# Kernel optimization log

Hardware: AMD Instinct MI355X
Metric: run time of the kernel (lower is better)

The kernel has to match this reference:

```python
import jax, jax.numpy as jnp
import numpy as np

B, N, DIM = 2, 2048, 1024
HEADS, DIM_HEAD = 16, 64
SCALE = DIM_HEAD ** 0.5  # NOTE: original code MULTIPLIES q by sqrt(d)


def setup_inputs() -> dict:
    key = jax.random.key(0)
    k1, k2, k3 = jax.random.split(key, 3)
    x = jax.random.normal(k1, (B, N, DIM), dtype=jnp.float32)
    mask = jnp.ones((B, N), dtype=bool)
    w_qkv = jax.random.normal(k2, (DIM, 3 * HEADS * DIM_HEAD), dtype=jnp.float32) * 0.02
    w_out = jax.random.normal(k3, (HEADS * DIM_HEAD, DIM), dtype=jnp.float32) * 0.02
    return {"x": x, "mask": mask, "w_qkv": w_qkv, "w_out": w_out}


def reference(x, mask, w_qkv, w_out):
    b, n, _ = x.shape
    # qkv projection: b n (qkv h d) -> qkv b h n d
    qkv = (x @ w_qkv).reshape(b, n, 3, HEADS, DIM_HEAD)
    qkv = jnp.transpose(qkv, (2, 0, 3, 1, 4))  # [3, b, h, n, d]
    q, k, v = qkv[0], qkv[1], qkv[2]
    q = q * SCALE
    sim = jnp.einsum('bhid,bhjd->bhij', q, k)
    neg = -jnp.finfo(sim.dtype).max
    sim = jnp.where(mask[:, None, None, :], sim, neg)
    attn = jax.nn.softmax(sim, axis=-1)
    out = jnp.einsum('bhij,bhjd->bhid', attn, v)  # [b, h, n, d]
    out = jnp.transpose(out, (0, 2, 1, 3)).reshape(b, n, HEADS * DIM_HEAD)
    return out @ w_out
```

## Files before the change

kernel.cpp:

```cpp
#include <hip/hip_runtime.h>
#include <hip/hip_bf16.h>

typedef _Float16 f16x8 __attribute__((ext_vector_type(8)));
typedef _Float16 f16x4 __attribute__((ext_vector_type(4)));
typedef float f32x4 __attribute__((ext_vector_type(4)));
typedef unsigned int u32;

#define MFMA16(a, b, c) __builtin_amdgcn_mfma_f32_16x16x32_f16(a, b, c, 0, 0, 0)

#define QSCALE 11.54156032f

__device__ __forceinline__ void gld16(const void* g, void* l) {
  using gp_t = const __attribute__((address_space(1))) u32*;
  using lp_t = __attribute__((address_space(3))) u32*;
  __builtin_amdgcn_global_load_lds((gp_t)g, (lp_t)l, 16, 0, 0);
}

__global__ void conv_f32_f16(const float* __restrict__ in, _Float16* __restrict__ out) {
  int i = (blockIdx.x * 256 + threadIdx.x) * 4;
  float4 v = *(const float4*)(in + i);
  f16x4 h = {(_Float16)v.x, (_Float16)v.y, (_Float16)v.z, (_Float16)v.w};
  *(f16x4*)(out + i) = h;
}

__global__ void transpose_f32_f16(const float* __restrict__ in, _Float16* __restrict__ out,
                                  int R, int C) {
  __shared__ float t[32][33];
  const int tx = threadIdx.x, ty = threadIdx.y;
  const int bx = blockIdx.x * 32, by = blockIdx.y * 32;
  for (int i = 0; i < 32; i += 8)
    t[ty + i][tx] = in[(size_t)(by + ty + i) * C + bx + tx];
  __syncthreads();
  for (int i = 0; i < 32; i += 8)
    out[(size_t)(bx + ty + i) * R + by + tx] = (_Float16)t[tx][ty + i];
}

template <int MODE>
__global__ __launch_bounds__(256) void gemm128(
    const _Float16* __restrict__ A, const _Float16* __restrict__ Bt, int Kd,
    _Float16* __restrict__ qo, _Float16* __restrict__ ko, _Float16* __restrict__ vt,
    float* __restrict__ fo, int Nd) {
  __shared__ __align__(16) _Float16 As[128 * 64];
  __shared__ __align__(16) _Float16 Bs[128 * 64];
  const int tid = threadIdx.x;
  const int w = tid >> 6, l = tid & 63;
  const int wm = w >> 1, wn = w & 1;
  const int lr = l & 15, lg = l >> 4;
  const int nwg = gridDim.x;
  int lin = blockIdx.x;
  lin = (lin & 7) * (nwg >> 3) + (lin >> 3);
  const int m0 = (lin & 31) * 128, n0 = (lin >> 5) * 128;

  const int srow = tid >> 3;
  const int scol = ((tid & 7) ^ (srow & 7)) * 8;
  const int swzr = (lr & 7) << 3;

  f32x4 acc[4][4];
  for (int i = 0; i < 4; ++i)
    for (int j = 0; j < 4; ++j) acc[i][j] = (f32x4){0.f, 0.f, 0.f, 0.f};

  const int NT = Kd >> 6;
  for (int kt = 0; kt < NT; ++kt) {
    const int k0 = kt * 64;
    for (int c = 0; c < 4; ++c) {
      const int row = c * 32 + srow;
      const int lbase = (c * 32 + w * 8) * 64;
      gld16(A + (size_t)(m0 + row) * Kd + k0 + scol, &As[lbase]);
      gld16(Bt + (size_t)(n0 + row) * Kd + k0 + scol, &Bs[lbase]);
    }
    __syncthreads();
    for (int kk = 0; kk < 2; ++kk) {
      f16x8 af[4], bf[4];
      const int cofs = (kk * 32 + lg * 8) ^ swzr;
      for (int mt = 0; mt < 4; ++mt)
        af[mt] = *(const f16x8*)&As[(wm * 64 + mt * 16 + lr) * 64 + cofs];
      for (int nt = 0; nt < 4; ++nt)
        bf[nt] = *(const f16x8*)&Bs[(wn * 64 + nt * 16 + lr) * 64 + cofs];
      for (int mt = 0; mt < 4; ++mt)
        for (int nt = 0; nt < 4; ++nt) acc[mt][nt] = MFMA16(af[mt], bf[nt], acc[mt][nt]);
    }
    __syncthreads();
  }

  for (int mt = 0; mt < 4; ++mt)
    for (int nt = 0; nt < 4; ++nt) {
      const int gmB = m0 + wm * 64 + mt * 16 + lg * 4;
      const int gn = n0 + wn * 64 + nt * 16 + lr;
      for (int r = 0; r < 4; ++r) {
        const int gm = gmB + r;
        const float v = acc[mt][nt][r];
        if (MODE == 0) {
          const int b = gm >> 11, ns = gm & 2047;
          const int sect = gn >> 10, rem = gn & 1023;
          const int h = rem >> 6, d = rem & 63;
          const size_t bh = (size_t)b * 16 + h;
          if (sect == 0)
            qo[(bh * 2048 + ns) * 64 + d] = (_Float16)(v * QSCALE);
          else if (sect == 1)
            ko[(bh * 2048 + ns) * 64 + d] = (_Float16)v;
          else
            vt[(bh * 64 + d) * 2048 + ns] = (_Float16)v;
        } else {
          fo[(size_t)gm * Nd + gn] = v;
        }
      }
    }
}

__global__ __launch_bounds__(256) void attn_kernel(
    const _Float16* __restrict__ Q, const _Float16* __restrict__ K,
    const _Float16* __restrict__ Vt, _Float16* __restrict__ AO) {
  __shared__ __align__(16) _Float16 Kls[64 * 64];
  __shared__ __align__(16) _Float16 Vls[64 * 64];
  __shared__ __align__(16) _Float16 Pls[4 * 16 * 64];
  const int qt = blockIdx.x, bh = blockIdx.y;
  const int b = bh >> 4, h = bh & 15;
  const int tid = threadIdx.x, w = tid >> 6, l = tid & 63;
  const int lr = l & 15, lg = l >> 4;
  const int q0 = qt * 64;
  const int pswz = (lr & 7) << 3;

  f16x8 qf[2];
  {
    const _Float16* qp = Q + ((size_t)bh * 2048 + q0 + w * 16 + lr) * 64 + lg * 8;
    qf[0] = *(const f16x8*)qp;
    qf[1] = *(const f16x8*)(qp + 32);
  }
  float mrun = -INFINITY, lsum = 0.f;
  f32x4 ao[4];
  for (int dt = 0; dt < 4; ++dt) ao[dt] = (f32x4){0.f, 0.f, 0.f, 0.f};

  const int srow = tid >> 2, cb = tid & 3;
  const _Float16* Kbase = K + ((size_t)bh * 2048 + srow) * 64 + cb * 8;
  const _Float16* Vbase = Vt + ((size_t)bh * 64 + srow) * 2048 + cb * 8;
  const int lofs0 = srow * 64 + ((cb ^ (srow & 7)) << 3);
  const int lofs1 = srow * 64 + (((cb + 4) ^ (srow & 7)) << 3);

  f16x8 kr0, kr1, vr0, vr1;
  kr0 = *(const f16x8*)(Kbase);
  kr1 = *(const f16x8*)(Kbase + 32);
  vr0 = *(const f16x8*)(Vbase);
  vr1 = *(const f16x8*)(Vbase + 32);
  *(f16x8*)&Kls[lofs0] = kr0;
  *(f16x8*)&Kls[lofs1] = kr1;
  *(f16x8*)&Vls[lofs0] = vr0;
  *(f16x8*)&Vls[lofs1] = vr1;
  __syncthreads();

  _Float16* pw = &Pls[w * (16 * 64)];
  const int NT = 2048 / 64;
  for (int t = 0; t < NT; ++t) {
    if (t + 1 < NT) {
      const size_t g = (size_t)(t + 1) * 64;
      kr0 = *(const f16x8*)(Kbase + g * 64);
      kr1 = *(const f16x8*)(Kbase + g * 64 + 32);
      vr0 = *(const f16x8*)(Vbase + g);
      vr1 = *(const f16x8*)(Vbase + g + 32);
    }
    f32x4 sc[4];
    for (int ct = 0; ct < 4; ++ct) sc[ct] = (f32x4){0.f, 0.f, 0.f, 0.f};
    __builtin_amdgcn_s_setprio(1);
    for (int ct = 0; ct < 4; ++ct)
      for (int kg = 0; kg < 2; ++kg) {
        f16x8 kf = *(const f16x8*)&Kls[(ct * 16 + lr) * 64 + ((kg * 32 + lg * 8) ^ pswz)];
        sc[ct] = MFMA16(kf, qf[kg], sc[ct]);
      }
    __builtin_amdgcn_s_setprio(0);
    float tm = fmaxf(fmaxf(fmaxf(sc[0][0], sc[0][1]), fmaxf(sc[0][2], sc[0][3])),
                     fmaxf(fmaxf(sc[1][0], sc[1][1]), fmaxf(sc[1][2], sc[1][3])));
    tm = fmaxf(tm, fmaxf(fmaxf(fmaxf(sc[2][0], sc[2][1]), fmaxf(sc[2][2], sc[2][3])),
                         fmaxf(fmaxf(sc[3][0], sc[3][1]), fmaxf(sc[3][2], sc[3][3]))));
    tm = fmaxf(tm, __shfl_xor(tm, 16));
    tm = fmaxf(tm, __shfl_xor(tm, 32));
    if (__any(tm > mrun)) {
      const float nm = fmaxf(mrun, tm);
      const float corr = exp2f(mrun - nm);
      mrun = nm;
      lsum *= corr;
      float cr[4];
      for (int r = 0; r < 4; ++r) cr[r] = __shfl(corr, lg * 4 + r);
      for (int dt = 0; dt < 4; ++dt)
        for (int r = 0; r < 4; ++r) ao[dt][r] *= cr[r];
    }
    float ps = 0.f;
    for (int ct = 0; ct < 4; ++ct) {
      f16x4 ph;
      for (int r = 0; r < 4; ++r) {
        const float p = exp2f(sc[ct][r] - mrun);
        ps += p;
        ph[r] = (_Float16)p;
      }
      *(f16x4*)&pw[lr * 64 + ((ct * 16 + lg * 4) ^ pswz)] = ph;
    }
    lsum += ps;
    f16x8 pf0 = *(const f16x8*)&pw[lr * 64 + ((lg * 8) ^ pswz)];
    f16x8 pf1 = *(const f16x8*)&pw[lr * 64 + ((32 + lg * 8) ^ pswz)];
    __builtin_amdgcn_s_setprio(1);
    for (int dt = 0; dt < 4; ++dt) {
      f16x8 vf0 = *(const f16x8*)&Vls[(dt * 16 + lr) * 64 + ((lg * 8) ^ pswz)];
      f16x8 vf1 = *(const f16x8*)&Vls[(dt * 16 + lr) * 64 + ((32 + lg * 8) ^ pswz)];
      ao[dt] = MFMA16(pf0, vf0, ao[dt]);
      ao[dt] = MFMA16(pf1, vf1, ao[dt]);
    }
    __builtin_amdgcn_s_setprio(0);
    __syncthreads();
    if (t + 1 < NT) {
      *(f16x8*)&Kls[lofs0] = kr0;
      *(f16x8*)&Kls[lofs1] = kr1;
      *(f16x8*)&Vls[lofs0] = vr0;
      *(f16x8*)&Vls[lofs1] = vr1;
      __syncthreads();
    }
  }
  lsum += __shfl_xor(lsum, 16);
  lsum += __shfl_xor(lsum, 32);
  const float inv = 1.f / lsum;
  float invr[4];
  for (int r = 0; r < 4; ++r) invr[r] = __shfl(inv, lg * 4 + r);
  for (int r = 0; r < 4; ++r) {
    const int row = q0 + w * 16 + lg * 4 + r;
    for (int dt = 0; dt < 4; ++dt) {
      const int col = h * 64 + dt * 16 + lr;
      AO[((size_t)b * 2048 + row) * 1024 + col] = (_Float16)(ao[dt][r] * invr[r]);
    }
  }
}

extern "C" void kernel_launch(void* const* d_in, const int* in_sizes, int n_in,
                              void* d_out, int out_size, void* d_ws, size_t ws_size,
                              hipStream_t stream) {
  const float* x = (const float*)d_in[0];
  const float* wqkv = (const float*)d_in[2];
  const float* wout = (const float*)d_in[3];
  float* out = (float*)d_out;

  _Float16* xb = (_Float16*)d_ws;
  _Float16* wqkvt = xb + (size_t)4096 * 1024;
  _Float16* woutt = wqkvt + (size_t)3072 * 1024;
  _Float16* q = woutt + (size_t)1024 * 1024;
  _Float16* k = q + (size_t)4194304;
  _Float16* vt = k + (size_t)4194304;
  _Float16* aobuf = vt + (size_t)4194304;

  conv_f32_f16<<<4096, 256, 0, stream>>>(x, xb);
  transpose_f32_f16<<<dim3(96, 32), dim3(32, 8), 0, stream>>>(wqkv, wqkvt, 1024, 3072);
  transpose_f32_f16<<<dim3(32, 32), dim3(32, 8), 0, stream>>>(wout, woutt, 1024, 1024);
  gemm128<0><<<768, 256, 0, stream>>>(xb, wqkvt, 1024, q, k, vt, nullptr, 3072);
  attn_kernel<<<dim3(32, 32), 256, 0, stream>>>(q, k, vt, aobuf);
  gemm128<1><<<256, 256, 0, stream>>>(aobuf, woutt, 1024, nullptr, nullptr, nullptr,
                                      out, 1024);
}
```

Baseline: 164.7 us.

## Fuse prep kernels, double-buffer output GEMM, load V fragments directly in attention

The three conversion and transpose launches are merged into one prep kernel to cut launch overhead. The output-projection GEMM gets a double-buffered LDS pipeline so the next K-tile's global-to-LDS loads overlap the current MFMAs. In attention, V fragments are now loaded straight from global memory into registers, and K uses a two-slot LDS buffer, which removes one barrier per tile. The trade-off is more global traffic for V and more registers, which may lower occupancy.

```diff
diff --git a/kernel.cpp b/kernel.cpp
--- a/kernel.cpp
+++ b/kernel.cpp
@@ -16,32 +16,46 @@
   __builtin_amdgcn_global_load_lds((gp_t)g, (lp_t)l, 16, 0, 0);
 }
 
-__global__ void conv_f32_f16(const float* __restrict__ in, _Float16* __restrict__ out) {
-  int i = (blockIdx.x * 256 + threadIdx.x) * 4;
-  float4 v = *(const float4*)(in + i);
-  f16x4 h = {(_Float16)v.x, (_Float16)v.y, (_Float16)v.z, (_Float16)v.w};
-  *(f16x4*)(out + i) = h;
-}
-
-__global__ void transpose_f32_f16(const float* __restrict__ in, _Float16* __restrict__ out,
-                                  int R, int C) {
+__global__ __launch_bounds__(256) void prep_kernel(
+    const float* __restrict__ x, _Float16* __restrict__ xb,
+    const float* __restrict__ wqkv, _Float16* __restrict__ wqkvt,
+    const float* __restrict__ wout, _Float16* __restrict__ woutt) {
   __shared__ float t[32][33];
-  const int tx = threadIdx.x, ty = threadIdx.y;
-  const int bx = blockIdx.x * 32, by = blockIdx.y * 32;
+  const int bid = blockIdx.x, tid = threadIdx.x;
+  if (bid < 4096) {
+    const int i = (bid * 256 + tid) * 4;
+    float4 v = *(const float4*)(x + i);
+    f16x4 h = {(_Float16)v.x, (_Float16)v.y, (_Float16)v.z, (_Float16)v.w};
+    *(f16x4*)(xb + i) = h;
+    return;
+  }
+  const float* in;
+  _Float16* out;
+  int C, bx, by;
+  if (bid < 7168) {
+    const int b2 = bid - 4096;
+    in = wqkv; out = wqkvt; C = 3072;
+    bx = (b2 % 96) * 32; by = (b2 / 96) * 32;
+  } else {
+    const int b2 = bid - 7168;
+    in = wout; out = woutt; C = 1024;
+    bx = (b2 & 31) * 32; by = (b2 >> 5) * 32;
+  }
+  const int tx = tid & 31, ty = tid >> 5;
   for (int i = 0; i < 32; i += 8)
     t[ty + i][tx] = in[(size_t)(by + ty + i) * C + bx + tx];
   __syncthreads();
   for (int i = 0; i < 32; i += 8)
-    out[(size_t)(bx + ty + i) * R + by + tx] = (_Float16)t[tx][ty + i];
-}
-
-template <int MODE>
+    out[(size_t)(bx + ty + i) * 1024 + by + tx] = (_Float16)t[tx][ty + i];
+}
+
+template <int MODE, int DBUF>
 __global__ __launch_bounds__(256) void gemm128(
     const _Float16* __restrict__ A, const _Float16* __restrict__ Bt, int Kd,
     _Float16* __restrict__ qo, _Float16* __restrict__ ko, _Float16* __restrict__ vt,
     float* __restrict__ fo, int Nd) {
-  __shared__ __align__(16) _Float16 As[128 * 64];
-  __shared__ __align__(16) _Float16 Bs[128 * 64];
+  __shared__ __align__(16) _Float16 As[(DBUF ? 2 : 1) * 128 * 64];
+  __shared__ __align__(16) _Float16 Bs[(DBUF ? 2 : 1) * 128 * 64];
   const int tid = threadIdx.x;
   const int w = tid >> 6, l = tid & 63;
   const int wm = w >> 1, wn = w & 1;
@@ -59,19 +73,19 @@
   for (int i = 0; i < 4; ++i)
     for (int j = 0; j < 4; ++j) acc[i][j] = (f32x4){0.f, 0.f, 0.f, 0.f};
 
-  const int NT = Kd >> 6;
-  for (int kt = 0; kt < NT; ++kt) {
+  auto stageAB = [&](int bsel, int kt) {
     const int k0 = kt * 64;
     for (int c = 0; c < 4; ++c) {
       const int row = c * 32 + srow;
-      const int lbase = (c * 32 + w * 8) * 64;
+      const int lbase = bsel * 8192 + (c * 32 + w * 8) * 64;
       gld16(A + (size_t)(m0 + row) * Kd + k0 + scol, &As[lbase]);
       gld16(Bt + (size_t)(n0 + row) * Kd + k0 + scol, &Bs[lbase]);
     }
-    __syncthreads();
+  };
+  auto compute = [&](int bsel) {
     for (int kk = 0; kk < 2; ++kk) {
       f16x8 af[4], bf[4];
-      const int cofs = (kk * 32 + lg * 8) ^ swzr;
+      const int cofs = bsel * 8192 + ((kk * 32 + lg * 8) ^ swzr);
       for (int mt = 0; mt < 4; ++mt)
         af[mt] = *(const f16x8*)&As[(wm * 64 + mt * 16 + lr) * 64 + cofs];
       for (int nt = 0; nt < 4; ++nt)
@@ -79,7 +93,25 @@
       for (int mt = 0; mt < 4; ++mt)
         for (int nt = 0; nt < 4; ++nt) acc[mt][nt] = MFMA16(af[mt], bf[nt], acc[mt][nt]);
     }
+  };
+
+  const int NT = Kd >> 6;
+  if constexpr (DBUF) {
+    stageAB(0, 0);
     __syncthreads();
+    for (int kt = 0; kt < NT; ++kt) {
+      const int c = kt & 1;
+      if (kt + 1 < NT) stageAB(c ^ 1, kt + 1);
+      compute(c);
+      __syncthreads();
+    }
+  } else {
+    for (int kt = 0; kt < NT; ++kt) {
+      stageAB(0, kt);
+      __syncthreads();
+      compute(0);
+      __syncthreads();
+    }
   }
 
   for (int mt = 0; mt < 4; ++mt)
@@ -110,8 +142,7 @@
 __global__ __launch_bounds__(256) void attn_kernel(
     const _Float16* __restrict__ Q, const _Float16* __restrict__ K,
     const _Float16* __restrict__ Vt, _Float16* __restrict__ AO) {
-  __shared__ __align__(16) _Float16 Kls[64 * 64];
-  __shared__ __align__(16) _Float16 Vls[64 * 64];
+  __shared__ __align__(16) _Float16 Kls[2][64 * 64];
   __shared__ __align__(16) _Float16 Pls[4 * 16 * 64];
   const int qt = blockIdx.x, bh = blockIdx.y;
   const int b = bh >> 4, h = bh & 15;
@@ -132,37 +163,38 @@
 
   const int srow = tid >> 2, cb = tid & 3;
   const _Float16* Kbase = K + ((size_t)bh * 2048 + srow) * 64 + cb * 8;
-  const _Float16* Vbase = Vt + ((size_t)bh * 64 + srow) * 2048 + cb * 8;
   const int lofs0 = srow * 64 + ((cb ^ (srow & 7)) << 3);
   const int lofs1 = srow * 64 + (((cb + 4) ^ (srow & 7)) << 3);
-
-  f16x8 kr0, kr1, vr0, vr1;
-  kr0 = *(const f16x8*)(Kbase);
-  kr1 = *(const f16x8*)(Kbase + 32);
-  vr0 = *(const f16x8*)(Vbase);
-  vr1 = *(const f16x8*)(Vbase + 32);
-  *(f16x8*)&Kls[lofs0] = kr0;
-  *(f16x8*)&Kls[lofs1] = kr1;
-  *(f16x8*)&Vls[lofs0] = vr0;
-  *(f16x8*)&Vls[lofs1] = vr1;
+  const _Float16* Vg = Vt + (size_t)bh * 64 * 2048;
+
+  f16x8 kr0 = *(const f16x8*)(Kbase);
+  f16x8 kr1 = *(const f16x8*)(Kbase + 32);
+  *(f16x8*)&Kls[0][lofs0] = kr0;
+  *(f16x8*)&Kls[0][lofs1] = kr1;
   __syncthreads();
 
   _Float16* pw = &Pls[w * (16 * 64)];
   const int NT = 2048 / 64;
   for (int t = 0; t < NT; ++t) {
+    const int c = t & 1;
+    const int kv0 = t * 64;
     if (t + 1 < NT) {
-      const size_t g = (size_t)(t + 1) * 64;
-      kr0 = *(const f16x8*)(Kbase + g * 64);
-      kr1 = *(const f16x8*)(Kbase + g * 64 + 32);
-      vr0 = *(const f16x8*)(Vbase + g);
-      vr1 = *(const f16x8*)(Vbase + g + 32);
+      kr0 = *(const f16x8*)(Kbase + (size_t)(t + 1) * 4096);
+      kr1 = *(const f16x8*)(Kbase + (size_t)(t + 1) * 4096 + 32);
+    }
+    f16x8 vf[8];
+    for (int dt = 0; dt < 4; ++dt) {
+      const _Float16* vp = Vg + (size_t)(dt * 16 + lr) * 2048 + kv0 + lg * 8;
+      vf[2 * dt] = *(const f16x8*)vp;
+      vf[2 * dt + 1] = *(const f16x8*)(vp + 32);
     }
     f32x4 sc[4];
     for (int ct = 0; ct < 4; ++ct) sc[ct] = (f32x4){0.f, 0.f, 0.f, 0.f};
     __builtin_amdgcn_s_setprio(1);
     for (int ct = 0; ct < 4; ++ct)
       for (int kg = 0; kg < 2; ++kg) {
-        f16x8 kf = *(const f16x8*)&Kls[(ct * 16 + lr) * 64 + ((kg * 32 + lg * 8) ^ pswz)];
+        f16x8 kf =
+            *(const f16x8*)&Kls[c][(ct * 16 + lr) * 64 + ((kg * 32 + lg * 8) ^ pswz)];
         sc[ct] = MFMA16(kf, qf[kg], sc[ct]);
       }
     __builtin_amdgcn_s_setprio(0);
@@ -197,18 +229,13 @@
     f16x8 pf1 = *(const f16x8*)&pw[lr * 64 + ((32 + lg * 8) ^ pswz)];
     __builtin_amdgcn_s_setprio(1);
     for (int dt = 0; dt < 4; ++dt) {
-      f16x8 vf0 = *(const f16x8*)&Vls[(dt * 16 + lr) * 64 + ((lg * 8) ^ pswz)];
-      f16x8 vf1 = *(const f16x8*)&Vls[(dt * 16 + lr) * 64 + ((32 + lg * 8) ^ pswz)];
-      ao[dt] = MFMA16(pf0, vf0, ao[dt]);
-      ao[dt] = MFMA16(pf1, vf1, ao[dt]);
+      ao[dt] = MFMA16(pf0, vf[2 * dt], ao[dt]);
+      ao[dt] = MFMA16(pf1, vf[2 * dt + 1], ao[dt]);
     }
     __builtin_amdgcn_s_setprio(0);
-    __syncthreads();
     if (t + 1 < NT) {
-      *(f16x8*)&Kls[lofs0] = kr0;
-      *(f16x8*)&Kls[lofs1] = kr1;
-      *(f16x8*)&Vls[lofs0] = vr0;
-      *(f16x8*)&Vls[lofs1] = vr1;
+      *(f16x8*)&Kls[c ^ 1][lofs0] = kr0;
+      *(f16x8*)&Kls[c ^ 1][lofs1] = kr1;
       __syncthreads();
     }
   }
@@ -242,11 +269,9 @@
   _Float16* vt = k + (size_t)4194304;
   _Float16* aobuf = vt + (size_t)4194304;
 
-  conv_f32_f16<<<4096, 256, 0, stream>>>(x, xb);
-  transpose_f32_f16<<<dim3(96, 32), dim3(32, 8), 0, stream>>>(wqkv, wqkvt, 1024, 3072);
-  transpose_f32_f16<<<dim3(32, 32), dim3(32, 8), 0, stream>>>(wout, woutt, 1024, 1024);
-  gemm128<0><<<768, 256, 0, stream>>>(xb, wqkvt, 1024, q, k, vt, nullptr, 3072);
+  prep_kernel<<<8192, 256, 0, stream>>>(x, xb, wqkv, wqkvt, wout, woutt);
+  gemm128<0, 0><<<768, 256, 0, stream>>>(xb, wqkvt, 1024, q, k, vt, nullptr, 3072);
   attn_kernel<<<dim3(32, 32), 256, 0, stream>>>(q, k, vt, aobuf);
-  gemm128<1><<<256, 256, 0, stream>>>(aobuf, woutt, 1024, nullptr, nullptr, nullptr,
-                                      out, 1024);
-}
+  gemm128<1, 1><<<256, 256, 0, stream>>>(aobuf, woutt, 1024, nullptr, nullptr, nullptr,
+                                         out, 1024);
+}
```

New measurement: 246.5 us. +49.7%, slower.
